# Optimization experiments

Hardware: AMD Instinct MI355X
Metric: run time of the kernel (lower is better)

Reference implementation:

```python
import jax, jax.numpy as jnp
import numpy as np

LAYERS = 2
HIDDEN = 512
FFN = 2048
HEADS = 8
IMG = (32, 64)
SLEN = IMG[0] * IMG[1]
BSZ = 2
KEY_DIM = HIDDEN // HEADS      # 64
V_DIM = HIDDEN * 2             # 1024
HEAD_SIZE = V_DIM // HEADS     # 128
SCALE_BASE = 512.0
SCALING = KEY_DIM ** (-0.5)
LN_EPS = 1e-5


def xpos_apply(x):
    # x: [..., L, d]  (XPOS rotary with length-dependent decay, downscale=False)
    L, d = x.shape[-2], x.shape[-1]
    half = d // 2
    base = (jnp.arange(0, d, 2, dtype=jnp.float32) + 0.4 * d) / (1.4 * d)  # [half]
    min_pos = -(L // 2)
    pos = jnp.arange(min_pos, L + min_pos, dtype=jnp.float32)              # [L]
    scale = base[None, :] ** (pos[:, None] / SCALE_BASE)                   # [L, half]
    inv_freq = 1.0 / (10000.0 ** (jnp.arange(half, dtype=jnp.float32) / half))
    sinusoid = jnp.arange(L, dtype=jnp.float32)[:, None] * inv_freq[None, :]  # [L, half]
    sin = jnp.repeat(jnp.sin(sinusoid) * scale, 2, axis=-1)                # [L, d]
    cos = jnp.repeat(jnp.cos(sinusoid) * scale, 2, axis=-1)                # [L, d]
    x1 = x[..., 0::2]
    x2 = x[..., 1::2]
    rot = jnp.stack([-x2, x1], axis=-1).reshape(x.shape)  # rotate_every_two
    return x * cos + rot * sin


def layer_norm(x, g, b):
    mu = jnp.mean(x, axis=-1, keepdims=True)
    var = jnp.mean(jnp.square(x - mu), axis=-1, keepdims=True)
    return (x - mu) * jax.lax.rsqrt(var + LN_EPS) * g + b


def attention(x, Wq, Wk, Wv, Wo):
    B, S, _ = x.shape
    q = (x @ Wq).reshape(B, S, HEADS, KEY_DIM).transpose(0, 2, 1, 3)   # [B,H,S,dk]
    k = (x @ Wk).reshape(B, S, HEADS, KEY_DIM).transpose(0, 2, 1, 3)
    v = (x @ Wv).reshape(B, S, HEADS, HEAD_SIZE).transpose(0, 2, 1, 3)  # [B,H,S,hs]
    q = xpos_apply(q)
    k = xpos_apply(k)
    scores = jnp.einsum('bhqd,bhkd->bhqk', q, k)
    att = jax.nn.softmax(scores.astype(jnp.float32), axis=-1).astype(scores.dtype)
    att = att * SCALING  # note: scaling applied AFTER softmax, as in the source
    out = jnp.einsum('bhqk,bhkv->bhqv', att, v)                          # [B,H,S,hs]
    out = out.transpose(0, 2, 1, 3).reshape(B, S, V_DIM)
    return out @ Wo


def setup_inputs() -> dict:
    key = jax.random.key(0)
    ks = jax.random.split(key, 8)
    p = lambda k, shp: jax.random.normal(k, shp, dtype=jnp.float32) * 0.02
    return {
        'x':  jax.random.normal(ks[0], (BSZ, SLEN, HIDDEN), dtype=jnp.float32),
        'Wq': p(ks[1], (LAYERS, HIDDEN, HIDDEN)),
        'Wk': p(ks[2], (LAYERS, HIDDEN, HIDDEN)),
        'Wv': p(ks[3], (LAYERS, HIDDEN, V_DIM)),
        'Wo': p(ks[4], (LAYERS, V_DIM, HIDDEN)),
        'W1': p(ks[5], (LAYERS, HIDDEN, FFN)),
        'b1': jnp.zeros((LAYERS, FFN), jnp.float32),
        'W2': p(ks[6], (LAYERS, FFN, HIDDEN)),
        'b2': jnp.zeros((LAYERS, HIDDEN), jnp.float32),
        'g1': jnp.ones((LAYERS, HIDDEN), jnp.float32),
        'be1': jnp.zeros((LAYERS, HIDDEN), jnp.float32),
        'g2': jnp.ones((LAYERS, HIDDEN), jnp.float32),
        'be2': jnp.zeros((LAYERS, HIDDEN), jnp.float32),
    }


def reference(x, Wq, Wk, Wv, Wo, W1, b1, W2, b2, g1, be1, g2, be2):
    for i in range(LAYERS):
        y = layer_norm(x + attention(x, Wq[i], Wk[i], Wv[i], Wo[i]), g1[i], be1[i])
        ffn = jax.nn.relu(y @ W1[i] + b1[i]) @ W2[i] + b2[i]
        x = layer_norm(y + ffn, g2[i], be2[i])
    return x.reshape(x.shape[0], IMG[0], IMG[1], x.shape[2])
```

## Files before the change

### kernel.cpp

```cpp
#include <hip/hip_runtime.h>
#include <hip/hip_bf16.h>
#include <math.h>

#define LAYERS 2
#define HIDDEN 512
#define FFN_DIM 2048
#define HEADS 8
#define SLEN 2048
#define BSZ 2
#define MROWS 4096
#define ATT_SCALING 0.125f
#define LN_EPS 1e-5f
#define SCALE_BASE 512.0f
#define LOG2E 1.4426950408889634f

typedef unsigned short u16;
typedef unsigned int u32;
typedef __attribute__((ext_vector_type(8))) short bf16x8;
typedef __attribute__((ext_vector_type(4))) float f32x4;
typedef __attribute__((ext_vector_type(16))) float f32x16;

__device__ __forceinline__ float bf2f(u16 u) {
    union { u32 i; float f; } v; v.i = ((u32)u) << 16; return v.f;
}
__device__ __forceinline__ u16 f2bf(float f) {
    union { float f; u32 i; } v; v.f = f;
    u32 r = v.i + 0x7FFFu + ((v.i >> 16) & 1u);
    return (u16)(r >> 16);
}
__device__ __forceinline__ u32 pk2bf(float a, float b) {
    union { __hip_bfloat162 h; u32 u; } v;
    v.h = __float22bfloat162_rn(make_float2(a, b));
    return v.u;
}
__device__ __forceinline__ u32 cvtpk(float a, float b) {
    u32 r;
    asm("v_cvt_pk_bf16_f32 %0, %1, %2" : "=v"(r) : "v"(a), "v"(b));
    return r;
}
__device__ __forceinline__ void async16(const void* g, void* l) {
    __builtin_amdgcn_global_load_lds((const __attribute__((address_space(1))) void*)g,
                                     (__attribute__((address_space(3))) void*)l, 16, 0, 0);
}

__global__ __launch_bounds__(256) void prep_kernel(const float* __restrict__ x,
                                                   const float* __restrict__ Wq,
                                                   const float* __restrict__ Wk,
                                                   const float* __restrict__ Wv,
                                                   const float* __restrict__ Wo,
                                                   const float* __restrict__ W1,
                                                   const float* __restrict__ W2,
                                                   char* __restrict__ w,
                                                   float* __restrict__ Af,
                                                   u16* __restrict__ Ab,
                                                   float2* __restrict__ tab) {
    const size_t MB1 = 1u << 20;
    const int bid = blockIdx.x;
    const int tid = threadIdx.x;
    __shared__ float t[32][33];

    if (bid < 7168) {
        int l = bid / 3584;
        int tt = bid % 3584;
        u16* WqkvT = (u16*)(w + 48 * MB1 + (size_t)l * 2 * MB1);
        u16* WoT   = (u16*)(w + 52 * MB1 + (size_t)l * 1 * MB1);
        u16* W1T   = (u16*)(w + 54 * MB1 + (size_t)l * 2 * MB1);
        u16* W2T   = (u16*)(w + 58 * MB1 + (size_t)l * 2 * MB1);
        const float* src; u16* dst; int K, N, tix;
        if (tt < 256)       { src = Wq + (size_t)l * 512 * 512;  dst = WqkvT;              K = 512;  N = 512;  tix = tt; }
        else if (tt < 512)  { src = Wk + (size_t)l * 512 * 512;  dst = WqkvT + 512 * 512;  K = 512;  N = 512;  tix = tt - 256; }
        else if (tt < 1024) { src = Wv + (size_t)l * 512 * 1024; dst = WqkvT + 1024 * 512; K = 512;  N = 1024; tix = tt - 512; }
        else if (tt < 1536) { src = Wo + (size_t)l * 1024 * 512; dst = WoT;                K = 1024; N = 512;  tix = tt - 1024; }
        else if (tt < 2560) { src = W1 + (size_t)l * 512 * 2048; dst = W1T;                K = 512;  N = 2048; tix = tt - 1536; }
        else                { src = W2 + (size_t)l * 2048 * 512; dst = W2T;                K = 2048; N = 512;  tix = tt - 2560; }
        int ntx = N >> 5;
        int n0 = (tix % ntx) * 32, k0 = (tix / ntx) * 32;
        int tx = tid & 31, ty = tid >> 5;
#pragma unroll
        for (int i = 0; i < 4; i++)
            t[ty + 8 * i][tx] = src[(size_t)(k0 + ty + 8 * i) * N + n0 + tx];
        __syncthreads();
#pragma unroll
        for (int i = 0; i < 4; i++)
            dst[(size_t)(n0 + ty + 8 * i) * K + k0 + tx] = f2bf(t[tx][ty + 8 * i]);
    } else if (bid < 9216) {
        int i = ((bid - 7168) * 256 + tid) * 4;
        float4 v = *(const float4*)(x + i);
        *(float4*)(Af + i) = v;
        uint2 p;
        p.x = pk2bf(v.x, v.y);
        p.y = pk2bf(v.z, v.w);
        *(uint2*)(Ab + i) = p;
    } else {
        int idx = (bid - 9216) * 256 + tid;
        int j = idx & 31;
        int s = idx >> 5;
        float base = (2.0f * j + 0.4f * 64.0f) / (1.4f * 64.0f);
        float pos = (float)(s - 1024);
        float scale = powf(base, pos / SCALE_BASE);
        float inv_freq = powf(10000.0f, -(float)j / 32.0f);
        float ang = (float)s * inv_freq;
        tab[idx] = make_float2(cosf(ang) * scale, sinf(ang) * scale);
    }
}

__global__ __launch_bounds__(256) void xpos_vtrans(u16* __restrict__ QKV,
                                                   const float2* __restrict__ tab,
                                                   u16* __restrict__ VT) {
    const int bid = blockIdx.x;
    const int tid = threadIdx.x;
    __shared__ u16 t[64][65];

    if (bid < 4096) {
        int idx = bid * 256 + tid;
        int j = idx & 31;
        int h = (idx >> 5) & 7;
        int s = (idx >> 8) & 2047;
        int b = idx >> 19;

        float2 cssn = tab[s * 32 + j];
        float cs = cssn.x, sn = cssn.y;

        size_t off = (size_t)(b * SLEN + s) * 2048 + h * 64 + 2 * j;
        u32* pq = (u32*)(QKV + off);
        u32* pk = (u32*)(QKV + off + 512);

        u32 qv = *pq;
        float q0 = bf2f((u16)(qv & 0xffff)), q1 = bf2f((u16)(qv >> 16));
        *pq = pk2bf((q0 * cs - q1 * sn) * LOG2E, (q1 * cs + q0 * sn) * LOG2E);

        u32 kv = *pk;
        float k0 = bf2f((u16)(kv & 0xffff)), k1 = bf2f((u16)(kv >> 16));
        *pk = pk2bf(k0 * cs - k1 * sn, k1 * cs + k0 * sn);
    } else {
        int v = bid - 4096;
        int bz = v & 15;
        int vy = (v >> 4) & 1;
        int sx = v >> 5;
        int b = bz >> 3, h = bz & 7;
        int s0 = sx * 64, v0 = vy * 64;
#pragma unroll
        for (int i = 0; i < 16; i++) {
            int e = tid + i * 256; int r = e >> 6, c = e & 63;
            t[r][c] = QKV[(size_t)(b * SLEN + s0 + r) * 2048 + 1024 + h * 128 + v0 + c];
        }
        __syncthreads();
#pragma unroll
        for (int i = 0; i < 16; i++) {
            int e = tid + i * 256; int r = e >> 6, c = e & 63;
            VT[(size_t)((b * 8 + h) * 128 + v0 + r) * 2048 + s0 + c] = t[c][r];
        }
    }
}

template <int BM, int BN, int BK, int WM, int OUTF32, int BIAS, int RELU, int NSPLIT>
__global__ __launch_bounds__(256) void gemm_mfma(const u16* __restrict__ A,
                                                 const u16* __restrict__ WT,
                                                 const float* __restrict__ bias,
                                                 void* __restrict__ C0,
                                                 void* __restrict__ C1,
                                                 int M, int N, int K) {
    constexpr int WN  = 4 / WM;
    constexpr int AM  = BM / (WM * 16);
    constexpr int AN  = BN / (WN * 16);
    constexpr int KO  = BK / 32;
    constexpr int AIT = BM * BK / 2048;
    constexpr int BIT = BN * BK / 2048;
    constexpr int KB8 = BK / 8;

    __shared__ u16 As[2][BM * BK];
    __shared__ u16 Bs[2][BN * BK];

    const int tid  = threadIdx.x;
    const int wave = tid >> 6;
    const int lane = tid & 63;
    const int quad = lane >> 4;
    const int l15  = lane & 15;
    const int wm = wave % WM;
    const int wn = wave / WM;

    const int tm = blockIdx.y * BM;
    const int tn = blockIdx.x * BN;
    const int z  = (NSPLIT > 1) ? blockIdx.z : 0;
    const int Ksub = K / NSPLIT;
    const int k0g  = z * Ksub;

    auto issue = [&](int kt, int buf) {
#pragma unroll
        for (int it = 0; it < AIT; it++) {
            int cid = it * 256 + tid;
            async16(A + (size_t)(tm + cid / KB8) * K + k0g + kt + (cid % KB8) * 8,
                    (char*)As[buf] + (it * 256 + wave * 64) * 16);
        }
#pragma unroll
        for (int it = 0; it < BIT; it++) {
            int cid = it * 256 + tid;
            async16(WT + (size_t)(tn + cid / KB8) * K + k0g + kt + (cid % KB8) * 8,
                    (char*)Bs[buf] + (it * 256 + wave * 64) * 16);
        }
    };

    f32x4 acc[AM][AN];
#pragma unroll
    for (int i = 0; i < AM; i++)
#pragma unroll
        for (int j = 0; j < AN; j++) acc[i][j] = (f32x4){0.f, 0.f, 0.f, 0.f};

    const int nk = Ksub / BK;
    issue(0, 0);

    for (int t = 0; t < nk; t++) {
        __syncthreads();
        if (t + 1 < nk) issue((t + 1) * BK, (t + 1) & 1);
        const int buf = t & 1;

        bf16x8 af[KO][AM], bfr[KO][AN];
#pragma unroll
        for (int ko = 0; ko < KO; ko++) {
#pragma unroll
            for (int i = 0; i < AM; i++)
                af[ko][i] = *(const bf16x8*)((const char*)As[buf] +
                    (((wm * (AM * 16) + i * 16 + l15) * KB8) + ko * 4 + quad) * 16);
#pragma unroll
            for (int j = 0; j < AN; j++)
                bfr[ko][j] = *(const bf16x8*)((const char*)Bs[buf] +
                    (((wn * (AN * 16) + j * 16 + l15) * KB8) + ko * 4 + quad) * 16);
        }
#pragma unroll
        for (int ko = 0; ko < KO; ko++)
#pragma unroll
            for (int i = 0; i < AM; i++)
#pragma unroll
                for (int j = 0; j < AN; j++)
                    acc[i][j] = __builtin_amdgcn_mfma_f32_16x16x32_bf16(
                        af[ko][i], bfr[ko][j], acc[i][j], 0, 0, 0);
    }

    void* Cout = (NSPLIT > 1 && z) ? C1 : C0;
#pragma unroll
    for (int i = 0; i < AM; i++) {
#pragma unroll
        for (int j = 0; j < AN; j++) {
            int col = tn + wn * (AN * 16) + j * 16 + l15;
            float bv = (BIAS && z == 0) ? bias[col] : 0.0f;
#pragma unroll
            for (int r = 0; r < 4; r++) {
                int row = tm + wm * (AM * 16) + i * 16 + quad * 4 + r;
                float v = acc[i][j][r] + bv;
                if (RELU) v = fmaxf(v, 0.0f);
                if (OUTF32) ((float*)Cout)[(size_t)row * N + col] = v;
                else        ((u16*)Cout)[(size_t)row * N + col] = f2bf(v);
            }
        }
    }
}

__global__ __launch_bounds__(256, 3) void flash_attn_mfma(const u16* __restrict__ QKV,
                                                          const u16* __restrict__ VT,
                                                          u16* __restrict__ OP0,
                                                          u16* __restrict__ OP1,
                                                          u16* __restrict__ OP2,
                                                          float* __restrict__ MLW) {
    const int h  = blockIdx.x;
    const int q0 = blockIdx.y * 128;
    const int bz = blockIdx.z;
    const int b  = bz / 3;
    const int split = bz - b * 3;
    const int tid  = threadIdx.x;
    const int wave = tid >> 6;
    const int lane = tid & 63;
    const int l31  = lane & 31;
    const int hi   = lane >> 5;
    const int swz  = (l31 & 7) ^ ((l31 >> 3) << 1);

    __shared__ u16 Ks[2][64 * 64];
    __shared__ u16 Vs[2][128 * 64];

    const int tcnt = (split == 2) ? 10 : 11;
    const int kb0  = split * 704;

    const u16* kp[2];
    const u16* vp[4];
#pragma unroll
    for (int it = 0; it < 2; it++) {
        int cid = it * 256 + tid;
        int row = cid >> 3;
        int lc  = (cid & 7) ^ (row & 7) ^ (((row >> 3) & 3) << 1);
        kp[it] = QKV + (size_t)(b * SLEN + kb0 + row) * 2048 + 512 + h * 64 + lc * 8;
    }
#pragma unroll
    for (int it = 0; it < 4; it++) {
        int cid = it * 256 + tid;
        int row = cid >> 3;
        int lc  = (cid & 7) ^ (row & 7) ^ (((row >> 3) & 3) << 1);
        vp[it] = VT + (size_t)((b * 8 + h) * 128 + row) * 2048 + kb0 + lc * 8;
    }

    auto issueKV = [&](int buf) {
#pragma unroll
        for (int it = 0; it < 2; it++) {
            async16(kp[it], (char*)Ks[buf] + (it * 256 + wave * 64) * 16);
            kp[it] += 64 * 2048;
        }
#pragma unroll
        for (int it = 0; it < 4; it++) {
            async16(vp[it], (char*)Vs[buf] + (it * 256 + wave * 64) * 16);
            vp[it] += 64;
        }
    };

    bf16x8 qf[4];
    {
        const u16* p = QKV + (size_t)(b * SLEN + q0 + wave * 32 + l31) * 2048 +
                       h * 64 + hi * 8;
#pragma unroll
        for (int dc = 0; dc < 4; dc++) qf[dc] = *(const bf16x8*)(p + dc * 16);
    }

    f32x16 o_acc[4];
#pragma unroll
    for (int rb = 0; rb < 4; rb++)
#pragma unroll
        for (int r = 0; r < 16; r++) o_acc[rb][r] = 0.f;
    float m = -1e30f;
    float l = 0.f;

    issueKV(0);

    for (int ti = 0; ti < tcnt; ti++) {
        __syncthreads();
        if (ti + 1 < tcnt) issueKV((ti + 1) & 1);
        const int buf = ti & 1;

        f32x16 st[2];
#pragma unroll
        for (int kb = 0; kb < 2; kb++)
#pragma unroll
            for (int r = 0; r < 16; r++) st[kb][r] = 0.f;
        __builtin_amdgcn_s_setprio(1);
#pragma unroll
        for (int dc = 0; dc < 4; dc++)
#pragma unroll
            for (int kb = 0; kb < 2; kb++) {
                bf16x8 kf = *(const bf16x8*)((const char*)Ks[buf] +
                    ((kb * 32 + l31) * 8 + ((dc * 2 + hi) ^ swz)) * 16);
                st[kb] = __builtin_amdgcn_mfma_f32_32x32x16_bf16(kf, qf[dc],
                                                                 st[kb], 0, 0, 0);
            }
        __builtin_amdgcn_s_setprio(0);

        float fm[16];
#pragma unroll
        for (int r = 0; r < 16; r++) fm[r] = fmaxf(st[0][r], st[1][r]);
#pragma unroll
        for (int s = 8; s > 0; s >>= 1)
#pragma unroll
            for (int r = 0; r < s; r++) fm[r] = fmaxf(fm[r], fm[r + s]);
        float mx = fmaxf(fm[0], __shfl_xor(fm[0], 32, 64));

        float mnew = fmaxf(m, mx);
        float alpha = exp2f(m - mnew);
        m = mnew;

        float s0 = 0.f, s1 = 0.f, s2 = 0.f, s3 = 0.f;
#pragma unroll
        for (int kb = 0; kb < 2; kb++)
#pragma unroll
            for (int r = 0; r < 16; r += 4) {
                float p0 = exp2f(st[kb][r + 0] - mnew);
                float p1 = exp2f(st[kb][r + 1] - mnew);
                float p2 = exp2f(st[kb][r + 2] - mnew);
                float p3 = exp2f(st[kb][r + 3] - mnew);
                st[kb][r + 0] = p0; st[kb][r + 1] = p1;
                st[kb][r + 2] = p2; st[kb][r + 3] = p3;
                s0 += p0; s1 += p1; s2 += p2; s3 += p3;
            }
        float ls = (s0 + s1) + (s2 + s3);
        ls += __shfl_xor(ls, 32, 64);
        l = l * alpha + ls;

#pragma unroll
        for (int rb = 0; rb < 4; rb++)
#pragma unroll
            for (int r = 0; r < 16; r++) o_acc[rb][r] *= alpha;

#pragma unroll
        for (int kc = 0; kc < 4; kc++) {
            const int kb = kc >> 1, o = (kc & 1) * 8;
            u32 a1 = cvtpk(st[kb][o + 0], st[kb][o + 1]);
            u32 b1 = cvtpk(st[kb][o + 4], st[kb][o + 5]);
            u32 a2 = cvtpk(st[kb][o + 2], st[kb][o + 3]);
            u32 b2 = cvtpk(st[kb][o + 6], st[kb][o + 7]);
            asm volatile("v_permlane32_swap_b32 %0, %1" : "+v"(a1), "+v"(b1));
            asm volatile("v_permlane32_swap_b32 %0, %1" : "+v"(a2), "+v"(b2));
            union { u32 u[4]; bf16x8 v; } pf;
            pf.u[0] = a1; pf.u[1] = a2; pf.u[2] = b1; pf.u[3] = b2;
            __builtin_amdgcn_s_setprio(1);
#pragma unroll
            for (int rb = 0; rb < 4; rb++) {
                bf16x8 vb = *(const bf16x8*)((const char*)Vs[buf] +
                    ((rb * 32 + l31) * 8 + ((kc * 2 + hi) ^ swz)) * 16);
                o_acc[rb] = __builtin_amdgcn_mfma_f32_32x32x16_bf16(vb, pf.v,
                                                                    o_acc[rb], 0, 0, 0);
            }
            __builtin_amdgcn_s_setprio(0);
        }
    }

    const int q = q0 + wave * 32 + l31;
    if (lane < 32)
        MLW[((size_t)(b * 3 + split) * 8 + h) * 2048 + q] = m + __log2f(l);
    const float invl = 1.0f / l;
    u16* OP = (split == 0) ? OP0 : ((split == 1) ? OP1 : OP2);
    const size_t rstride = (split == 2) ? 2048 : 1024;
    size_t rowbase = ((size_t)(b * SLEN + q)) * rstride + h * 128;
#pragma unroll
    for (int rb = 0; rb < 4; rb++)
#pragma unroll
        for (int i = 0; i < 8; i++) {
            int v = rb * 32 + ((2 * i) & 3) + 8 * (i >> 1) + 4 * hi;
            *(u32*)(OP + rowbase + v) =
                pk2bf(o_acc[rb][2 * i] * invl, o_acc[rb][2 * i + 1] * invl);
        }
}

__global__ __launch_bounds__(256) void attn_combine(const u16* __restrict__ P0,
                                                    const u16* __restrict__ P1,
                                                    const u16* __restrict__ P2,
                                                    const float* __restrict__ MLW,
                                                    u16* __restrict__ AT) {
    int idx = (blockIdx.x * 256 + threadIdx.x) * 8;
    int col = idx & 1023;
    int row = idx >> 10;
    int h = col >> 7;
    int b = row >> 11, q = row & 2047;
    float g0 = MLW[((size_t)(b * 3 + 0) * 8 + h) * 2048 + q];
    float g1 = MLW[((size_t)(b * 3 + 1) * 8 + h) * 2048 + q];
    float g2 = MLW[((size_t)(b * 3 + 2) * 8 + h) * 2048 + q];
    float M = fmaxf(g0, fmaxf(g1, g2));
    float e0 = exp2f(g0 - M), e1 = exp2f(g1 - M), e2 = exp2f(g2 - M);
    float norm = ATT_SCALING / (e0 + e1 + e2);
    e0 *= norm; e1 *= norm; e2 *= norm;

    uint4 a = *(const uint4*)(P0 + idx);
    uint4 c = *(const uint4*)(P1 + idx);
    uint4 d = *(const uint4*)(P2 + (size_t)row * 2048 + col);
    uint4 o;
    u32 au[4] = {a.x, a.y, a.z, a.w};
    u32 cu[4] = {c.x, c.y, c.z, c.w};
    u32 du[4] = {d.x, d.y, d.z, d.w};
    u32 ou[4];
#pragma unroll
    for (int k = 0; k < 4; k++) {
        float r0 = bf2f((u16)(au[k] & 0xffff)) * e0 + bf2f((u16)(cu[k] & 0xffff)) * e1 +
                   bf2f((u16)(du[k] & 0xffff)) * e2;
        float r1 = bf2f((u16)(au[k] >> 16)) * e0 + bf2f((u16)(cu[k] >> 16)) * e1 +
                   bf2f((u16)(du[k] >> 16)) * e2;
        ou[k] = pk2bf(r0, r1);
    }
    o.x = ou[0]; o.y = ou[1]; o.z = ou[2]; o.w = ou[3];
    *(uint4*)(AT + idx) = o;
}

__global__ __launch_bounds__(256) void addln_kernel(const float* __restrict__ X,
                                                    const float* __restrict__ R0,
                                                    const float* __restrict__ R1,
                                                    const float* __restrict__ g,
                                                    const float* __restrict__ be,
                                                    float* __restrict__ dstf,
                                                    u16* __restrict__ dstb) {
    const int row = blockIdx.x;
    const int tid = threadIdx.x;
    __shared__ float red[256];
    size_t off = (size_t)row * HIDDEN + 2 * tid;
    float2 a  = *(const float2*)(X + off);
    float2 r0 = *(const float2*)(R0 + off);
    float2 r1 = *(const float2*)(R1 + off);
    float v0 = a.x + r0.x + r1.x;
    float v1 = a.y + r0.y + r1.y;
    red[tid] = v0 + v1;
    __syncthreads();
    for (int s = 128; s > 0; s >>= 1) { if (tid < s) red[tid] += red[tid + s]; __syncthreads(); }
    float mu = red[0] * (1.0f / HIDDEN);
    __syncthreads();
    float d0 = v0 - mu, d1 = v1 - mu;
    red[tid] = d0 * d0 + d1 * d1;
    __syncthreads();
    for (int s = 128; s > 0; s >>= 1) { if (tid < s) red[tid] += red[tid + s]; __syncthreads(); }
    float rstd = rsqrtf(red[0] * (1.0f / HIDDEN) + LN_EPS);
    float2 gg = *(const float2*)(g + 2 * tid);
    float2 bb = *(const float2*)(be + 2 * tid);
    float o0 = d0 * rstd * gg.x + bb.x;
    float o1 = d1 * rstd * gg.y + bb.y;
    *(float2*)(dstf + off) = make_float2(o0, o1);
    *(u32*)(dstb + off) = pk2bf(o0, o1);
}

extern "C" void kernel_launch(void* const* d_in, const int* in_sizes, int n_in,
                              void* d_out, int out_size, void* d_ws, size_t ws_size,
                              hipStream_t stream) {
    const float* x   = (const float*)d_in[0];
    const float* Wq  = (const float*)d_in[1];
    const float* Wk  = (const float*)d_in[2];
    const float* Wv  = (const float*)d_in[3];
    const float* Wo  = (const float*)d_in[4];
    const float* W1  = (const float*)d_in[5];
    const float* b1  = (const float*)d_in[6];
    const float* W2  = (const float*)d_in[7];
    const float* b2  = (const float*)d_in[8];
    const float* g1  = (const float*)d_in[9];
    const float* be1 = (const float*)d_in[10];
    const float* g2  = (const float*)d_in[11];
    const float* be2 = (const float*)d_in[12];
    float* out = (float*)d_out;

    const size_t MB = 1u << 20;
    char* w = (char*)d_ws;
    float*  R1f  = (float*)(w);
    float*  F2a  = (float*)(w);
    u16*    VTg  = (u16*)(w + 8 * MB);
    float*  Yf   = (float*)(w + 8 * MB);
    u16*    OP1  = (u16*)(w + 16 * MB);
    float*  PfA  = (float*)(w + 16 * MB);
    float*  F2b  = (float*)(w + 16 * MB);
    u16*    QKV  = (u16*)(w + 24 * MB);
    float*  PfB  = (float*)(w + 24 * MB);
    u16*    F1   = (u16*)(w + 24 * MB);
    u16*    A_bf = (u16*)(w + 40 * MB);
    u16*    OP0  = (u16*)(w + 40 * MB);
    u16*    AT   = (u16*)(w + 40 * MB);
    u16*    Y_bf = (u16*)(w + 40 * MB);
    float2* xtab = (float2*)(w + 62 * MB);
    float*  MLW  = (float*)(w + 62 * MB + 512 * 1024);
    u16*    OP2  = QKV + 1024;

    prep_kernel<<<9472, 256, 0, stream>>>(x, Wq, Wk, Wv, Wo, W1, W2,
                                          w, R1f, A_bf, xtab);

    for (int l = 0; l < LAYERS; l++) {
        u16* WqkvT = (u16*)(w + 48 * MB + (size_t)l * 2 * MB);
        u16* WoT   = (u16*)(w + 52 * MB + (size_t)l * 1 * MB);
        u16* W1T   = (u16*)(w + 54 * MB + (size_t)l * 2 * MB);
        u16* W2T   = (u16*)(w + 58 * MB + (size_t)l * 2 * MB);
        const float* b1_l  = b1 + (size_t)l * FFN_DIM;
        const float* b2_l  = b2 + (size_t)l * HIDDEN;
        const float* g1_l  = g1 + (size_t)l * HIDDEN;
        const float* be1_l = be1 + (size_t)l * HIDDEN;
        const float* g2_l  = g2 + (size_t)l * HIDDEN;
        const float* be2_l = be2 + (size_t)l * HIDDEN;

        gemm_mfma<128, 128, 64, 2, 0, 0, 0, 1><<<dim3(16, 32), 256, 0, stream>>>(
            A_bf, WqkvT, nullptr, QKV, nullptr, MROWS, 2048, 512);

        xpos_vtrans<<<5120, 256, 0, stream>>>(QKV, xtab, VTg);

        flash_attn_mfma<<<dim3(8, 16, 6), 256, 0, stream>>>(QKV, VTg, OP0, OP1,
                                                            OP2, MLW);
        attn_combine<<<MROWS * 1024 / 2048, 256, 0, stream>>>(OP0, OP1, OP2,
                                                              MLW, AT);

        gemm_mfma<128, 64, 64, 2, 1, 0, 0, 2><<<dim3(8, 32, 2), 256, 0, stream>>>(
            AT, WoT, nullptr, PfA, PfB, MROWS, 512, 1024);

        addln_kernel<<<MROWS, 256, 0, stream>>>(R1f, PfA, PfB, g1_l, be1_l, Yf, Y_bf);

        gemm_mfma<128, 128, 64, 2, 0, 1, 1, 1><<<dim3(16, 32), 256, 0, stream>>>(
            Y_bf, W1T, b1_l, F1, nullptr, MROWS, 2048, 512);

        gemm_mfma<128, 64, 64, 2, 1, 1, 0, 2><<<dim3(8, 32, 2), 256, 0, stream>>>(
            F1, W2T, b2_l, F2a, F2b, MROWS, 512, 2048);

        float* dstf = (l == LAYERS - 1) ? out : R1f;
        addln_kernel<<<MROWS, 256, 0, stream>>>(Yf, F2a, F2b, g2_l, be2_l, dstf, A_bf);
    }
}
```

Baseline: 404.3 us.

## Shrink GEMM K-tile, add occupancy bounds, and use wave-per-row LayerNorm

New measurement: 402.6 us. About the same (-0.4%).

```diff
diff --git a/kernel.cpp b/kernel.cpp
--- a/kernel.cpp
+++ b/kernel.cpp
@@ -153,8 +153,9 @@
     }
 }
 
-template <int BM, int BN, int BK, int WM, int OUTF32, int BIAS, int RELU, int NSPLIT>
-__global__ __launch_bounds__(256) void gemm_mfma(const u16* __restrict__ A,
+template <int BM, int BN, int BK, int WM, int OUTF32, int BIAS, int RELU,
+          int NSPLIT, int WPE>
+__global__ __launch_bounds__(256, WPE) void gemm_mfma(const u16* __restrict__ A,
                                                  const u16* __restrict__ WT,
                                                  const float* __restrict__ bias,
                                                  void* __restrict__ C0,
@@ -469,31 +470,47 @@
                                                     const float* __restrict__ be,
                                                     float* __restrict__ dstf,
                                                     u16* __restrict__ dstb) {
-    const int row = blockIdx.x;
-    const int tid = threadIdx.x;
-    __shared__ float red[256];
-    size_t off = (size_t)row * HIDDEN + 2 * tid;
-    float2 a  = *(const float2*)(X + off);
-    float2 r0 = *(const float2*)(R0 + off);
-    float2 r1 = *(const float2*)(R1 + off);
-    float v0 = a.x + r0.x + r1.x;
-    float v1 = a.y + r0.y + r1.y;
-    red[tid] = v0 + v1;
-    __syncthreads();
-    for (int s = 128; s > 0; s >>= 1) { if (tid < s) red[tid] += red[tid + s]; __syncthreads(); }
-    float mu = red[0] * (1.0f / HIDDEN);
-    __syncthreads();
-    float d0 = v0 - mu, d1 = v1 - mu;
-    red[tid] = d0 * d0 + d1 * d1;
-    __syncthreads();
-    for (int s = 128; s > 0; s >>= 1) { if (tid < s) red[tid] += red[tid + s]; __syncthreads(); }
-    float rstd = rsqrtf(red[0] * (1.0f / HIDDEN) + LN_EPS);
-    float2 gg = *(const float2*)(g + 2 * tid);
-    float2 bb = *(const float2*)(be + 2 * tid);
-    float o0 = d0 * rstd * gg.x + bb.x;
-    float o1 = d1 * rstd * gg.y + bb.y;
-    *(float2*)(dstf + off) = make_float2(o0, o1);
-    *(u32*)(dstb + off) = pk2bf(o0, o1);
+    const int tid  = threadIdx.x;
+    const int wave = tid >> 6;
+    const int lane = tid & 63;
+    const int row  = blockIdx.x * 4 + wave;
+    size_t off = (size_t)row * HIDDEN + lane * 8;
+
+    float4 a0 = *(const float4*)(X + off),  a1 = *(const float4*)(X + off + 4);
+    float4 p0 = *(const float4*)(R0 + off), p1 = *(const float4*)(R0 + off + 4);
+    float4 q0 = *(const float4*)(R1 + off), q1 = *(const float4*)(R1 + off + 4);
+    float v[8];
+    v[0] = a0.x + p0.x + q0.x; v[1] = a0.y + p0.y + q0.y;
+    v[2] = a0.z + p0.z + q0.z; v[3] = a0.w + p0.w + q0.w;
+    v[4] = a1.x + p1.x + q1.x; v[5] = a1.y + p1.y + q1.y;
+    v[6] = a1.z + p1.z + q1.z; v[7] = a1.w + p1.w + q1.w;
+
+    float s = ((v[0] + v[1]) + (v[2] + v[3])) + ((v[4] + v[5]) + (v[6] + v[7]));
+#pragma unroll
+    for (int d = 1; d < 64; d <<= 1) s += __shfl_xor(s, d, 64);
+    float mu = s * (1.0f / HIDDEN);
+
+    float t = 0.f;
+#pragma unroll
+    for (int j = 0; j < 8; j++) { float dv = v[j] - mu; v[j] = dv; t += dv * dv; }
+#pragma unroll
+    for (int d = 1; d < 64; d <<= 1) t += __shfl_xor(t, d, 64);
+    float rstd = rsqrtf(t * (1.0f / HIDDEN) + LN_EPS);
+
+    float4 g0 = *(const float4*)(g + lane * 8),  g1 = *(const float4*)(g + lane * 8 + 4);
+    float4 b0 = *(const float4*)(be + lane * 8), b1 = *(const float4*)(be + lane * 8 + 4);
+    float o[8];
+    o[0] = v[0] * rstd * g0.x + b0.x; o[1] = v[1] * rstd * g0.y + b0.y;
+    o[2] = v[2] * rstd * g0.z + b0.z; o[3] = v[3] * rstd * g0.w + b0.w;
+    o[4] = v[4] * rstd * g1.x + b1.x; o[5] = v[5] * rstd * g1.y + b1.y;
+    o[6] = v[6] * rstd * g1.z + b1.z; o[7] = v[7] * rstd * g1.w + b1.w;
+
+    *(float4*)(dstf + off)     = make_float4(o[0], o[1], o[2], o[3]);
+    *(float4*)(dstf + off + 4) = make_float4(o[4], o[5], o[6], o[7]);
+    uint4 ob;
+    ob.x = pk2bf(o[0], o[1]); ob.y = pk2bf(o[2], o[3]);
+    ob.z = pk2bf(o[4], o[5]); ob.w = pk2bf(o[6], o[7]);
+    *(uint4*)(dstb + off) = ob;
 }
 
 extern "C" void kernel_launch(void* const* d_in, const int* in_sizes, int n_in,
@@ -549,7 +566,7 @@
         const float* g2_l  = g2 + (size_t)l * HIDDEN;
         const float* be2_l = be2 + (size_t)l * HIDDEN;
 
-        gemm_mfma<128, 128, 64, 2, 0, 0, 0, 1><<<dim3(16, 32), 256, 0, stream>>>(
+        gemm_mfma<128, 128, 32, 2, 0, 0, 0, 1, 4><<<dim3(16, 32), 256, 0, stream>>>(
             A_bf, WqkvT, nullptr, QKV, nullptr, MROWS, 2048, 512);
 
         xpos_vtrans<<<5120, 256, 0, stream>>>(QKV, xtab, VTg);
@@ -559,18 +576,18 @@
         attn_combine<<<MROWS * 1024 / 2048, 256, 0, stream>>>(OP0, OP1, OP2,
                                                               MLW, AT);
 
-        gemm_mfma<128, 64, 64, 2, 1, 0, 0, 2><<<dim3(8, 32, 2), 256, 0, stream>>>(
+        gemm_mfma<128, 64, 32, 2, 1, 0, 0, 2, 4><<<dim3(8, 32, 2), 256, 0, stream>>>(
             AT, WoT, nullptr, PfA, PfB, MROWS, 512, 1024);
 
-        addln_kernel<<<MROWS, 256, 0, stream>>>(R1f, PfA, PfB, g1_l, be1_l, Yf, Y_bf);
-
-        gemm_mfma<128, 128, 64, 2, 0, 1, 1, 1><<<dim3(16, 32), 256, 0, stream>>>(
+        addln_kernel<<<MROWS / 4, 256, 0, stream>>>(R1f, PfA, PfB, g1_l, be1_l, Yf, Y_bf);
+
+        gemm_mfma<128, 128, 32, 2, 0, 1, 1, 1, 4><<<dim3(16, 32), 256, 0, stream>>>(
             Y_bf, W1T, b1_l, F1, nullptr, MROWS, 2048, 512);
 
-        gemm_mfma<128, 64, 64, 2, 1, 1, 0, 2><<<dim3(8, 32, 2), 256, 0, stream>>>(
+        gemm_mfma<128, 64, 32, 2, 1, 1, 0, 2, 4><<<dim3(8, 32, 2), 256, 0, stream>>>(
             F1, W2T, b2_l, F2a, F2b, MROWS, 512, 2048);
 
         float* dstf = (l == LAYERS - 1) ? out : R1f;
-        addln_kernel<<<MROWS, 256, 0, stream>>>(Yf, F2a, F2b, g2_l, be2_l, dstf, A_bf);
-    }
-}
+        addln_kernel<<<MROWS / 4, 256, 0, stream>>>(Yf, F2a, F2b, g2_l, be2_l, dstf, A_bf);
+    }
+}
```
